# Kernel optimization log

Hardware: AMD Instinct MI355X
Metric: run time of the kernel (lower is better)

Reference implementation:

```python
import jax, jax.numpy as jnp
import numpy as np
import math

NUM_HEADS = 16
D_MODEL = 1024
LN_EPS = 1e-5


def _layer_norm(x, g, b):
    mu = jnp.mean(x, axis=-1, keepdims=True)
    var = jnp.mean((x - mu) ** 2, axis=-1, keepdims=True)
    return (x - mu) / jnp.sqrt(var + LN_EPS) * g + b


def setup_inputs() -> dict:
    key = jax.random.key(0)
    ks = jax.random.split(key, 12)
    B, H, W, d = 32, 16, 16, D_MODEL
    P, F = 64, 128
    s = 0.02
    return {
        "x": jax.random.normal(ks[0], (B, H, W, d), jnp.float32),
        "pattern_features": jax.random.normal(ks[1], (B, P, F), jnp.float32),
        "wq": jax.random.normal(ks[2], (d, d), jnp.float32) * s,
        "bq": jnp.zeros((d,), jnp.float32),
        "wk": jax.random.normal(ks[3], (d, d), jnp.float32) * s,
        "bk": jnp.zeros((d,), jnp.float32),
        "wv": jax.random.normal(ks[4], (d, d), jnp.float32) * s,
        "bv": jnp.zeros((d,), jnp.float32),
        "wo": jax.random.normal(ks[5], (d, d), jnp.float32) * s,
        "bo": jnp.zeros((d,), jnp.float32),
        "ln_g": jnp.ones((d,), jnp.float32),
        "ln_b": jnp.zeros((d,), jnp.float32),
    }


def reference(x, pattern_features, wq, bq, wk, bk, wv, bv, wo, bo, ln_g, ln_b):
    B, H, W, d = x.shape
    S = H * W
    nh = NUM_HEADS
    dk = d // nh
    x_seq = x.reshape(B, S, d)

    def proj(w, b):
        return (x_seq @ w.T + b).reshape(B, S, nh, dk).transpose(0, 2, 1, 3)  # (B,nh,S,dk)

    q, k, v = proj(wq, bq), proj(wk, bk), proj(wv, bv)
    scores = jnp.einsum("bhsd,bhtd->bhst", q, k) / math.sqrt(dk)  # (B,nh,S,S)

    # creative bias: diversity bonus on top-left min(S,64) block, same for all heads
    m = min(S, 64)
    sim = jnp.einsum("bpf,bqf->bpq", pattern_features, pattern_features)
    div = 1.0 - jax.nn.softmax(sim, axis=-1)  # (B,P,P)
    bias = jnp.zeros((B, nh, S, S), x.dtype)
    bias = bias.at[:, :, :m, :m].set(div[:, None, :m, :m] * 0.1)

    # faithful to torch: scores + bias.unsqueeze(0) -> rank-5 (1,B,nh,S,S)
    scores5 = scores[None] + bias[None]
    aw = jax.nn.softmax(scores5, axis=-1)
    attn = jnp.matmul(aw, v)  # (1,B,nh,S,dk) via broadcasting
    # faithful to torch transpose(1,2).view(B,S,d): row-major reshape of (1,nh,B,S,dk)
    attn = jnp.transpose(attn, (0, 2, 1, 3, 4)).reshape(B, S, d)

    out = attn @ wo.T + bo
    out = _layer_norm(out + x_seq, ln_g, ln_b)

    attention_weights = jax.nn.softmax(scores, axis=-1).mean(axis=1)  # (B,S,S)
    return out.reshape(B, H, W, d), attention_weights
```

## Files before the change

kernel.cpp:

```cpp
#include <hip/hip_runtime.h>

typedef unsigned short u16;
typedef unsigned int   u32;
typedef short bf16x8 __attribute__((ext_vector_type(8)));
typedef float f32x4  __attribute__((ext_vector_type(4)));

__device__ __forceinline__ float bf2f(u16 u){
  union { u32 u; float f; } c; c.u = ((u32)u) << 16; return c.f;
}
__device__ __forceinline__ u16 f2bf(float f){
  union { float f; u32 u; } c; c.f = f;
  u32 u = c.u + 0x7fffu + ((c.u >> 16) & 1u);
  return (u16)(u >> 16);
}

__device__ __forceinline__ void gload16(const u16* g, u16* l){
  __builtin_amdgcn_global_load_lds((const __attribute__((address_space(1))) u32*)g,
                                   (__attribute__((address_space(3))) u32*)l, 16, 0, 0);
}

__device__ __forceinline__ float waveRed(float v, int ismax){
  #pragma unroll
  for (int o = 32; o > 0; o >>= 1){
    float t = __shfl_xor(v, o, 64);
    v = ismax ? fmaxf(v, t) : (v + t);
  }
  return v;
}
__device__ __forceinline__ float blockRed(float v, int ismax, float* red, int tid){
  v = waveRed(v, ismax);
  __syncthreads();
  if ((tid & 63) == 0) red[tid >> 6] = v;
  __syncthreads();
  return ismax ? fmaxf(fmaxf(red[0], red[1]), fmaxf(red[2], red[3]))
               : (red[0] + red[1] + red[2] + red[3]);
}

__global__ __launch_bounds__(256)
void conv_x(const float* __restrict__ src, u16* __restrict__ dst){
  const size_t i = ((size_t)blockIdx.x * 256 + threadIdx.x) * 8;
  const float4 a = *(const float4*)(src + i);
  const float4 b = *(const float4*)(src + i + 4);
  uint4 o;
  o.x = (u32)f2bf(a.x) | ((u32)f2bf(a.y) << 16);
  o.y = (u32)f2bf(a.z) | ((u32)f2bf(a.w) << 16);
  o.z = (u32)f2bf(b.x) | ((u32)f2bf(b.y) << 16);
  o.w = (u32)f2bf(b.z) | ((u32)f2bf(b.w) << 16);
  *(uint4*)(dst + i) = o;
}

__global__ __launch_bounds__(256)
void conv_w4(const float* __restrict__ w0, const float* __restrict__ w1,
             const float* __restrict__ w2, const float* __restrict__ w3,
             u16* __restrict__ dst){
  const float* s = blockIdx.y == 0 ? w0 : (blockIdx.y == 1 ? w1 : (blockIdx.y == 2 ? w2 : w3));
  u16* d = dst + (size_t)blockIdx.y * 1048576;
  const size_t i = ((size_t)blockIdx.x * 256 + threadIdx.x) * 8;
  const float4 a = *(const float4*)(s + i);
  const float4 b = *(const float4*)(s + i + 4);
  uint4 o;
  o.x = (u32)f2bf(a.x) | ((u32)f2bf(a.y) << 16);
  o.y = (u32)f2bf(a.z) | ((u32)f2bf(a.w) << 16);
  o.z = (u32)f2bf(b.x) | ((u32)f2bf(b.y) << 16);
  o.w = (u32)f2bf(b.z) | ((u32)f2bf(b.w) << 16);
  *(uint4*)(d + i) = o;
}

__global__ __launch_bounds__(256)
void div_kernel(const float* __restrict__ pf, float* __restrict__ divp)
{
  __shared__ float pfs[64][129];
  __shared__ float svs[64][65];
  const int b = blockIdx.x;
  const int tid = threadIdx.x;
  const float* pb = pf + (size_t)b * 8192;
  for (int i = tid; i < 8192; i += 256) pfs[i >> 7][i & 127] = pb[i];
  __syncthreads();
  const int p = tid & 63, qg = tid >> 6;
  for (int qq = qg * 16; qq < qg * 16 + 16; ++qq){
    float a = 0.f;
    #pragma unroll 8
    for (int f = 0; f < 128; ++f) a += pfs[p][f] * pfs[qq][f];
    svs[p][qq] = a;
  }
  __syncthreads();
  if (tid < 64){
    float m = -1e30f;
    for (int qq = 0; qq < 64; ++qq) m = fmaxf(m, svs[tid][qq]);
    float s = 0.f;
    for (int qq = 0; qq < 64; ++qq){ const float e = __expf(svs[tid][qq] - m); svs[tid][qq] = e; s += e; }
    const float inv = 1.f / s;
    float* dr = divp + ((size_t)b * 64 + tid) * 64;
    for (int qq = 0; qq < 64; ++qq) dr[qq] = 0.1f * (1.f - svs[tid][qq] * inv);
  }
}

template<int MODE>
__global__ __launch_bounds__(256)
void gemm_lds(const u16* __restrict__ A, const u16* __restrict__ Wb,
              const float* __restrict__ bias0, const float* __restrict__ bias1,
              const float* __restrict__ bias2, void* __restrict__ outp)
{
  __shared__ u16 As[128 * 32];
  __shared__ u16 Bs[128 * 32];
  const int tid = threadIdx.x, lane = tid & 63, w = tid >> 6;
  const int wm = (w >> 1) * 64, wn = (w & 1) * 64;
  const int bm = blockIdx.x;
  int bn = blockIdx.y;
  const u16* Wp = Wb;
  const float* bias = bias0;
  float scale = 1.f;
  int wsel = 0;
  if (MODE == 0){
    wsel = bn >> 3; bn &= 7;
    Wp = Wb + (size_t)wsel * 1048576;
    bias = wsel == 0 ? bias0 : (wsel == 1 ? bias1 : bias2);
    if (wsel == 0) scale = 0.125f;
  }

  const f32x4 z = {0.f, 0.f, 0.f, 0.f};
  f32x4 acc[4][4];
  #pragma unroll
  for (int i = 0; i < 4; ++i)
    #pragma unroll
    for (int j = 0; j < 4; ++j) acc[i][j] = z;

  const int r4 = lane >> 2, c8 = (lane & 3) * 8;
  const int ca0 = w * 2, ca1 = w * 2 + 1;
  const u16* ga0 = A  + (size_t)(bm * 128 + ca0 * 16 + r4) * 1024 + c8;
  const u16* ga1 = A  + (size_t)(bm * 128 + ca1 * 16 + r4) * 1024 + c8;
  const u16* gb0 = Wp + (size_t)(bn * 128 + ca0 * 16 + r4) * 1024 + c8;
  const u16* gb1 = Wp + (size_t)(bn * 128 + ca1 * 16 + r4) * 1024 + c8;
  u16* la0 = As + ca0 * 512 + lane * 8;
  u16* la1 = As + ca1 * 512 + lane * 8;
  u16* lb0 = Bs + ca0 * 512 + lane * 8;
  u16* lb1 = Bs + ca1 * 512 + lane * 8;

  const int fr = lane & 15, q8 = (lane >> 4) * 8;
  for (int k0 = 0; k0 < 1024; k0 += 32){
    __syncthreads();
    gload16(ga0 + k0, la0);
    gload16(ga1 + k0, la1);
    gload16(gb0 + k0, lb0);
    gload16(gb1 + k0, lb1);
    __syncthreads();
    bf16x8 af[4], bfv[4];
    #pragma unroll
    for (int i = 0; i < 4; ++i) af[i]  = *(const bf16x8*)&As[(wm + i * 16 + fr) * 32 + q8];
    #pragma unroll
    for (int j = 0; j < 4; ++j) bfv[j] = *(const bf16x8*)&Bs[(wn + j * 16 + fr) * 32 + q8];
    #pragma unroll
    for (int i = 0; i < 4; ++i)
      #pragma unroll
      for (int j = 0; j < 4; ++j)
        acc[i][j] = __builtin_amdgcn_mfma_f32_16x16x32_bf16(af[i], bfv[j], acc[i][j], 0, 0, 0);
  }

  #pragma unroll
  for (int i = 0; i < 4; ++i){
    #pragma unroll
    for (int j = 0; j < 4; ++j){
      const int gr0 = bm * 128 + wm + i * 16 + ((lane >> 4) * 4);
      const int gc  = bn * 128 + wn + j * 16 + (lane & 15);
      const float bvv = bias[gc];
      #pragma unroll
      for (int r = 0; r < 4; ++r){
        const int gr = gr0 + r;
        const float val = (acc[i][j][r] + bvv) * scale;
        if (MODE == 0){
          const int b = gr >> 8, s = gr & 255, h = gc >> 6, kk = gc & 63;
          ((u16*)outp)[(size_t)wsel * 8388608 + (size_t)b * 262144 +
                       (size_t)h * 16384 + (size_t)s * 64 + kk] = f2bf(val);
        } else {
          ((float*)outp)[(size_t)gr * 1024 + gc] = val;
        }
      }
    }
  }
}

__global__ __launch_bounds__(256)
void attn_mfma(const u16* __restrict__ q, const u16* __restrict__ k,
               const u16* __restrict__ v, const float* __restrict__ divp,
               u16* __restrict__ attn_s)
{
  __shared__ u16 Vt[64][264];
  __shared__ u16 Ps[4][16][136];
  const int bh = blockIdx.x;
  const int b = bh >> 4, h = bh & 15;
  const int tid = threadIdx.x, lane = tid & 63, w = tid >> 6;
  const int quad = lane >> 4, l15 = lane & 15;
  const u16* kh = k + (size_t)bh * 16384;
  const u16* vh = v + (size_t)bh * 16384;
  const u16* qh = q + (size_t)bh * 16384;

  #pragma unroll
  for (int c = 0; c < 4; ++c){
    const int pidx = tid + c * 256;
    const int t2 = pidx & 127;
    const int n0 = (pidx >> 7) * 8;
    const uint4 a  = *(const uint4*)(vh + (2 * t2) * 64 + n0);
    const uint4 bb = *(const uint4*)(vh + (2 * t2 + 1) * 64 + n0);
    const u32 aa[4] = {a.x, a.y, a.z, a.w};
    const u32 bb4[4] = {bb.x, bb.y, bb.z, bb.w};
    #pragma unroll
    for (int j2 = 0; j2 < 4; ++j2){
      const u32 lo = aa[j2], hi = bb4[j2];
      *(u32*)&Vt[n0 + 2 * j2    ][2 * t2] = (lo & 0xffffu) | (hi << 16);
      *(u32*)&Vt[n0 + 2 * j2 + 1][2 * t2] = (lo >> 16) | (hi & 0xffff0000u);
    }
  }
  __syncthreads();

  const f32x4 z = {0.f, 0.f, 0.f, 0.f};
  const int bp = 2 * h + (b >> 4);
  for (int i = 0; i < 4; ++i){
    const int row0 = w * 64 + i * 16;
    const bf16x8 af0 = *(const bf16x8*)(qh + (size_t)(row0 + l15) * 64 + quad * 8);
    const bf16x8 af1 = *(const bf16x8*)(qh + (size_t)(row0 + l15) * 64 + 32 + quad * 8);
    f32x4 sc[16];
    #pragma unroll
    for (int ct = 0; ct < 16; ++ct){
      const bf16x8 b0 = *(const bf16x8*)(kh + (size_t)(ct * 16 + l15) * 64 + quad * 8);
      const bf16x8 b1 = *(const bf16x8*)(kh + (size_t)(ct * 16 + l15) * 64 + 32 + quad * 8);
      f32x4 a = __builtin_amdgcn_mfma_f32_16x16x32_bf16(af0, b0, z, 0, 0, 0);
      sc[ct]  = __builtin_amdgcn_mfma_f32_16x16x32_bf16(af1, b1, a, 0, 0, 0);
    }
    if (w == 0){
      const float* dv = divp + (size_t)b * 4096 + (size_t)(i * 16 + quad * 4) * 64 + l15;
      #pragma unroll
      for (int ct = 0; ct < 4; ++ct)
        #pragma unroll
        for (int rr = 0; rr < 4; ++rr)
          sc[ct][rr] += dv[rr * 64 + ct * 16];
    }
    float rs[4];
    #pragma unroll
    for (int rr = 0; rr < 4; ++rr){
      float m = sc[0][rr];
      #pragma unroll
      for (int ct = 1; ct < 16; ++ct) m = fmaxf(m, sc[ct][rr]);
      #pragma unroll
      for (int o = 1; o < 16; o <<= 1) m = fmaxf(m, __shfl_xor(m, o, 64));
      float s = 0.f;
      #pragma unroll
      for (int ct = 0; ct < 16; ++ct){
        const float e = __expf(sc[ct][rr] - m); sc[ct][rr] = e; s += e;
      }
      #pragma unroll
      for (int o = 1; o < 16; o <<= 1) s += __shfl_xor(s, o, 64);
      rs[rr] = 1.f / s;
    }
    f32x4 o4[4] = {z, z, z, z};
    #pragma unroll
    for (int half = 0; half < 2; ++half){
      #pragma unroll
      for (int ct = 0; ct < 8; ++ct)
        #pragma unroll
        for (int rr = 0; rr < 4; ++rr)
          Ps[w][quad * 4 + rr][ct * 16 + l15] = f2bf(sc[half * 8 + ct][rr] * rs[rr]);
      #pragma unroll
      for (int kc = 0; kc < 4; ++kc){
        const bf16x8 pa = *(const bf16x8*)&Ps[w][l15][kc * 32 + quad * 8];
        #pragma unroll
        for (int nt = 0; nt < 4; ++nt){
          const bf16x8 vb8 = *(const bf16x8*)&Vt[nt * 16 + l15][half * 128 + kc * 32 + quad * 8];
          o4[nt] = __builtin_amdgcn_mfma_f32_16x16x32_bf16(pa, vb8, o4[nt], 0, 0, 0);
        }
      }
    }
    const int sp = (b & 15) * 16 + (w * 4 + i);
    #pragma unroll
    for (int nt = 0; nt < 4; ++nt)
      #pragma unroll
      for (int rr = 0; rr < 4; ++rr){
        const int slo = quad * 4 + rr;
        const int cp = slo * 64 + nt * 16 + l15;
        attn_s[((size_t)bp * 256 + sp) * 1024 + cp] = f2bf(o4[nt][rr]);
      }
  }
}

__global__ __launch_bounds__(256)
void aw_kernel(const u16* __restrict__ q, const u16* __restrict__ k,
               float* __restrict__ aw)
{
  __shared__ float redm[16][4];
  __shared__ float reds[16][4];
  const int blk = blockIdx.x;
  const int b = blk >> 4, st = blk & 15;
  const int tid = threadIdx.x, lane = tid & 63, w = tid >> 6;
  const int quad = lane >> 4, l15 = lane & 15;
  const int rowb = st * 16;
  const f32x4 z = {0.f, 0.f, 0.f, 0.f};
  float awacc[4][4] = {};
  for (int h = 0; h < 16; ++h){
    const u16* kh = k + (((size_t)b * 16 + h) * 16384);
    const u16* qh = q + (((size_t)b * 16 + h) * 16384);
    const bf16x8 af0 = *(const bf16x8*)(qh + (size_t)(rowb + l15) * 64 + quad * 8);
    const bf16x8 af1 = *(const bf16x8*)(qh + (size_t)(rowb + l15) * 64 + 32 + quad * 8);
    f32x4 sc[4];
    #pragma unroll
    for (int j4 = 0; j4 < 4; ++j4){
      const int ct = w * 4 + j4;
      const bf16x8 b0 = *(const bf16x8*)(kh + (size_t)(ct * 16 + l15) * 64 + quad * 8);
      const bf16x8 b1 = *(const bf16x8*)(kh + (size_t)(ct * 16 + l15) * 64 + 32 + quad * 8);
      f32x4 a = __builtin_amdgcn_mfma_f32_16x16x32_bf16(af0, b0, z, 0, 0, 0);
      sc[j4]  = __builtin_amdgcn_mfma_f32_16x16x32_bf16(af1, b1, a, 0, 0, 0);
    }
    float pm[4];
    #pragma unroll
    for (int rr = 0; rr < 4; ++rr){
      float m = fmaxf(fmaxf(sc[0][rr], sc[1][rr]), fmaxf(sc[2][rr], sc[3][rr]));
      #pragma unroll
      for (int o = 1; o < 16; o <<= 1) m = fmaxf(m, __shfl_xor(m, o, 64));
      pm[rr] = m;
    }
    if (l15 == 0)
      #pragma unroll
      for (int rr = 0; rr < 4; ++rr) redm[quad * 4 + rr][w] = pm[rr];
    __syncthreads();
    float ps[4];
    #pragma unroll
    for (int rr = 0; rr < 4; ++rr){
      const int row = quad * 4 + rr;
      const float m = fmaxf(fmaxf(redm[row][0], redm[row][1]),
                            fmaxf(redm[row][2], redm[row][3]));
      float s = 0.f;
      #pragma unroll
      for (int j4 = 0; j4 < 4; ++j4){
        const float e = __expf(sc[j4][rr] - m); sc[j4][rr] = e; s += e;
      }
      #pragma unroll
      for (int o = 1; o < 16; o <<= 1) s += __shfl_xor(s, o, 64);
      ps[rr] = s;
    }
    if (l15 == 0)
      #pragma unroll
      for (int rr = 0; rr < 4; ++rr) reds[quad * 4 + rr][w] = ps[rr];
    __syncthreads();
    #pragma unroll
    for (int rr = 0; rr < 4; ++rr){
      const int row = quad * 4 + rr;
      const float inv = 1.f / (reds[row][0] + reds[row][1] + reds[row][2] + reds[row][3]);
      #pragma unroll
      for (int j4 = 0; j4 < 4; ++j4) awacc[j4][rr] += sc[j4][rr] * inv;
    }
  }
  const size_t base = (size_t)b * 65536;
  #pragma unroll
  for (int j4 = 0; j4 < 4; ++j4){
    const int col = (w * 4 + j4) * 16 + l15;
    #pragma unroll
    for (int rr = 0; rr < 4; ++rr){
      const int row = rowb + quad * 4 + rr;
      aw[base + (size_t)row * 256 + col] = awacc[j4][rr] * 0.0625f;
    }
  }
}

__global__ __launch_bounds__(256)
void ln_kernel(const float* __restrict__ y2, const float* __restrict__ x,
               const float* __restrict__ g, const float* __restrict__ bb,
               float* __restrict__ outp)
{
  __shared__ float red[4];
  const int r = blockIdx.x, tid = threadIdx.x;
  const float4 yv = ((const float4*)(y2 + (size_t)r * 1024))[tid];
  const float4 xv = ((const float4*)(x  + (size_t)r * 1024))[tid];
  const float v0 = yv.x + xv.x;
  const float v1 = yv.y + xv.y;
  const float v2 = yv.z + xv.z;
  const float v3 = yv.w + xv.w;
  const float ssum = blockRed(v0 + v1 + v2 + v3, 0, red, tid);
  const float mu = ssum * (1.f / 1024.f);
  const float d0 = v0 - mu, d1 = v1 - mu, d2 = v2 - mu, d3 = v3 - mu;
  const float sq = blockRed(d0 * d0 + d1 * d1 + d2 * d2 + d3 * d3, 0, red, tid);
  const float rstd = rsqrtf(sq * (1.f / 1024.f) + 1e-5f);
  const float4 gv = ((const float4*)g)[tid];
  const float4 bv = ((const float4*)bb)[tid];
  float4 o;
  o.x = d0 * rstd * gv.x + bv.x;
  o.y = d1 * rstd * gv.y + bv.y;
  o.z = d2 * rstd * gv.z + bv.z;
  o.w = d3 * rstd * gv.w + bv.w;
  ((float4*)(outp + (size_t)r * 1024))[tid] = o;
}

extern "C" void kernel_launch(void* const* d_in, const int* in_sizes, int n_in,
                              void* d_out, int out_size, void* d_ws, size_t ws_size,
                              hipStream_t stream)
{
  int ix = -1, ipf = -1, iw[4] = {-1,-1,-1,-1}, iv[6] = {-1,-1,-1,-1,-1,-1};
  int nw = 0, nv = 0;
  for (int i = 0; i < n_in; ++i){
    const int sz = in_sizes[i];
    if (sz == 8388608 && ix < 0) ix = i;
    else if (sz == 262144 && ipf < 0) ipf = i;
    else if (sz == 1048576 && nw < 4) iw[nw++] = i;
    else if (sz == 1024 && nv < 6) iv[nv++] = i;
  }
  if (ix < 0 || ipf < 0 || nw != 4 || nv != 6){
    ix = 0; ipf = 1; iw[0] = 2; iv[0] = 3; iw[1] = 4; iv[1] = 5;
    iw[2] = 6; iv[2] = 7; iw[3] = 8; iv[3] = 9; iv[4] = 10; iv[5] = 11;
  }

  const float* x   = (const float*)d_in[ix];
  const float* pf  = (const float*)d_in[ipf];
  const float* wq  = (const float*)d_in[iw[0]];
  const float* wk  = (const float*)d_in[iw[1]];
  const float* wv  = (const float*)d_in[iw[2]];
  const float* wo  = (const float*)d_in[iw[3]];
  const float* bq  = (const float*)d_in[iv[0]];
  const float* bk  = (const float*)d_in[iv[1]];
  const float* bv  = (const float*)d_in[iv[2]];
  const float* bo  = (const float*)d_in[iv[3]];
  const float* lng = (const float*)d_in[iv[4]];
  const float* lnb = (const float*)d_in[iv[5]];

  float* out0   = (float*)d_out;
  float* aw_out = out0 + 8388608;

  u16* x_bf = (u16*)d_out;
  u16* attn = x_bf + 8388608;
  u16* qkv    = (u16*)d_ws;
  float* divp = (float*)((char*)d_ws + (size_t)48 * 1048576);
  u16* warena = (u16*)((char*)d_ws + (size_t)49 * 1048576);
  float* y2   = (float*)d_ws;

  conv_x<<<4096, 256, 0, stream>>>(x, x_bf);
  conv_w4<<<dim3(512, 4), 256, 0, stream>>>(wq, wk, wv, wo, warena);
  div_kernel<<<32, 256, 0, stream>>>(pf, divp);

  gemm_lds<0><<<dim3(64, 24), 256, 0, stream>>>(x_bf, warena, bq, bk, bv, (void*)qkv);

  u16* qw = qkv, *kw = qkv + 8388608, *vw = qkv + 16777216;
  attn_mfma<<<512, 256, 0, stream>>>(qw, kw, vw, divp, attn);
  aw_kernel<<<512, 256, 0, stream>>>(qw, kw, aw_out);

  gemm_lds<1><<<dim3(64, 8), 256, 0, stream>>>(attn, warena + 3145728, bo, nullptr, nullptr, (void*)y2);
  ln_kernel<<<8192, 256, 0, stream>>>(y2, x, lng, lnb, out0);
}
```

Measured before the change: 330.8 us.

## Split attention blocks by row quarter and give each aw wave its own heads

The attention kernel now launches four blocks per (batch, head), each handling 64 query rows, instead of one block looping over 256 rows. This raises the grid from 512 to 2048 blocks for better CU occupancy, at the cost of each block redundantly transposing the full V tile into LDS. The averaged-weights kernel now has each wave process four heads over all 256 columns, which removes the per-head block-wide barriers. Per-wave partial sums are then combined through a 64KB LDS buffer, which may lower occupancy and raises register use (64 accumulators plus 64 score registers).

```diff
diff --git a/kernel.cpp b/kernel.cpp
--- a/kernel.cpp
+++ b/kernel.cpp
@@ -186,7 +186,8 @@
 {
   __shared__ u16 Vt[64][264];
   __shared__ u16 Ps[4][16][136];
-  const int bh = blockIdx.x;
+  const int blk = blockIdx.x;
+  const int bh = blk >> 2, rq = blk & 3;
   const int b = bh >> 4, h = bh & 15;
   const int tid = threadIdx.x, lane = tid & 63, w = tid >> 6;
   const int quad = lane >> 4, l15 = lane & 15;
@@ -214,148 +215,128 @@
 
   const f32x4 z = {0.f, 0.f, 0.f, 0.f};
   const int bp = 2 * h + (b >> 4);
-  for (int i = 0; i < 4; ++i){
-    const int row0 = w * 64 + i * 16;
-    const bf16x8 af0 = *(const bf16x8*)(qh + (size_t)(row0 + l15) * 64 + quad * 8);
-    const bf16x8 af1 = *(const bf16x8*)(qh + (size_t)(row0 + l15) * 64 + 32 + quad * 8);
-    f32x4 sc[16];
+  const int row0 = rq * 64 + w * 16;
+  const bf16x8 af0 = *(const bf16x8*)(qh + (size_t)(row0 + l15) * 64 + quad * 8);
+  const bf16x8 af1 = *(const bf16x8*)(qh + (size_t)(row0 + l15) * 64 + 32 + quad * 8);
+  f32x4 sc[16];
+  #pragma unroll
+  for (int ct = 0; ct < 16; ++ct){
+    const bf16x8 b0 = *(const bf16x8*)(kh + (size_t)(ct * 16 + l15) * 64 + quad * 8);
+    const bf16x8 b1 = *(const bf16x8*)(kh + (size_t)(ct * 16 + l15) * 64 + 32 + quad * 8);
+    f32x4 a = __builtin_amdgcn_mfma_f32_16x16x32_bf16(af0, b0, z, 0, 0, 0);
+    sc[ct]  = __builtin_amdgcn_mfma_f32_16x16x32_bf16(af1, b1, a, 0, 0, 0);
+  }
+  if (rq == 0){
+    const float* dv = divp + (size_t)b * 4096 + (size_t)(w * 16 + quad * 4) * 64 + l15;
+    #pragma unroll
+    for (int ct = 0; ct < 4; ++ct)
+      #pragma unroll
+      for (int rr = 0; rr < 4; ++rr)
+        sc[ct][rr] += dv[rr * 64 + ct * 16];
+  }
+  float rs[4];
+  #pragma unroll
+  for (int rr = 0; rr < 4; ++rr){
+    float m = sc[0][rr];
+    #pragma unroll
+    for (int ct = 1; ct < 16; ++ct) m = fmaxf(m, sc[ct][rr]);
+    #pragma unroll
+    for (int o = 1; o < 16; o <<= 1) m = fmaxf(m, __shfl_xor(m, o, 64));
+    float s = 0.f;
     #pragma unroll
     for (int ct = 0; ct < 16; ++ct){
-      const bf16x8 b0 = *(const bf16x8*)(kh + (size_t)(ct * 16 + l15) * 64 + quad * 8);
-      const bf16x8 b1 = *(const bf16x8*)(kh + (size_t)(ct * 16 + l15) * 64 + 32 + quad * 8);
-      f32x4 a = __builtin_amdgcn_mfma_f32_16x16x32_bf16(af0, b0, z, 0, 0, 0);
-      sc[ct]  = __builtin_amdgcn_mfma_f32_16x16x32_bf16(af1, b1, a, 0, 0, 0);
-    }
-    if (w == 0){
-      const float* dv = divp + (size_t)b * 4096 + (size_t)(i * 16 + quad * 4) * 64 + l15;
-      #pragma unroll
-      for (int ct = 0; ct < 4; ++ct)
-        #pragma unroll
-        for (int rr = 0; rr < 4; ++rr)
-          sc[ct][rr] += dv[rr * 64 + ct * 16];
-    }
-    float rs[4];
+      const float e = __expf(sc[ct][rr] - m); sc[ct][rr] = e; s += e;
+    }
+    #pragma unroll
+    for (int o = 1; o < 16; o <<= 1) s += __shfl_xor(s, o, 64);
+    rs[rr] = 1.f / s;
+  }
+  f32x4 o4[4] = {z, z, z, z};
+  #pragma unroll
+  for (int half = 0; half < 2; ++half){
+    #pragma unroll
+    for (int ct = 0; ct < 8; ++ct)
+      #pragma unroll
+      for (int rr = 0; rr < 4; ++rr)
+        Ps[w][quad * 4 + rr][ct * 16 + l15] = f2bf(sc[half * 8 + ct][rr] * rs[rr]);
+    #pragma unroll
+    for (int kc = 0; kc < 4; ++kc){
+      const bf16x8 pa = *(const bf16x8*)&Ps[w][l15][kc * 32 + quad * 8];
+      #pragma unroll
+      for (int nt = 0; nt < 4; ++nt){
+        const bf16x8 vb8 = *(const bf16x8*)&Vt[nt * 16 + l15][half * 128 + kc * 32 + quad * 8];
+        o4[nt] = __builtin_amdgcn_mfma_f32_16x16x32_bf16(pa, vb8, o4[nt], 0, 0, 0);
+      }
+    }
+  }
+  const int sp = (b & 15) * 16 + rq * 4 + w;
+  #pragma unroll
+  for (int nt = 0; nt < 4; ++nt)
     #pragma unroll
     for (int rr = 0; rr < 4; ++rr){
-      float m = sc[0][rr];
-      #pragma unroll
-      for (int ct = 1; ct < 16; ++ct) m = fmaxf(m, sc[ct][rr]);
-      #pragma unroll
-      for (int o = 1; o < 16; o <<= 1) m = fmaxf(m, __shfl_xor(m, o, 64));
-      float s = 0.f;
-      #pragma unroll
-      for (int ct = 0; ct < 16; ++ct){
-        const float e = __expf(sc[ct][rr] - m); sc[ct][rr] = e; s += e;
-      }
-      #pragma unroll
-      for (int o = 1; o < 16; o <<= 1) s += __shfl_xor(s, o, 64);
-      rs[rr] = 1.f / s;
-    }
-    f32x4 o4[4] = {z, z, z, z};
-    #pragma unroll
-    for (int half = 0; half < 2; ++half){
-      #pragma unroll
-      for (int ct = 0; ct < 8; ++ct)
-        #pragma unroll
-        for (int rr = 0; rr < 4; ++rr)
-          Ps[w][quad * 4 + rr][ct * 16 + l15] = f2bf(sc[half * 8 + ct][rr] * rs[rr]);
-      #pragma unroll
-      for (int kc = 0; kc < 4; ++kc){
-        const bf16x8 pa = *(const bf16x8*)&Ps[w][l15][kc * 32 + quad * 8];
-        #pragma unroll
-        for (int nt = 0; nt < 4; ++nt){
-          const bf16x8 vb8 = *(const bf16x8*)&Vt[nt * 16 + l15][half * 128 + kc * 32 + quad * 8];
-          o4[nt] = __builtin_amdgcn_mfma_f32_16x16x32_bf16(pa, vb8, o4[nt], 0, 0, 0);
-        }
-      }
-    }
-    const int sp = (b & 15) * 16 + (w * 4 + i);
-    #pragma unroll
-    for (int nt = 0; nt < 4; ++nt)
-      #pragma unroll
-      for (int rr = 0; rr < 4; ++rr){
-        const int slo = quad * 4 + rr;
-        const int cp = slo * 64 + nt * 16 + l15;
-        attn_s[((size_t)bp * 256 + sp) * 1024 + cp] = f2bf(o4[nt][rr]);
-      }
-  }
+      const int slo = quad * 4 + rr;
+      const int cp = slo * 64 + nt * 16 + l15;
+      attn_s[((size_t)bp * 256 + sp) * 1024 + cp] = f2bf(o4[nt][rr]);
+    }
 }
 
 __global__ __launch_bounds__(256)
 void aw_kernel(const u16* __restrict__ q, const u16* __restrict__ k,
                float* __restrict__ aw)
 {
-  __shared__ float redm[16][4];
-  __shared__ float reds[16][4];
+  __shared__ float Ws[4][16][258];
   const int blk = blockIdx.x;
   const int b = blk >> 4, st = blk & 15;
   const int tid = threadIdx.x, lane = tid & 63, w = tid >> 6;
   const int quad = lane >> 4, l15 = lane & 15;
   const int rowb = st * 16;
   const f32x4 z = {0.f, 0.f, 0.f, 0.f};
-  float awacc[4][4] = {};
-  for (int h = 0; h < 16; ++h){
+  float awacc[16][4] = {};
+  #pragma unroll
+  for (int hh = 0; hh < 4; ++hh){
+    const int h = w * 4 + hh;
     const u16* kh = k + (((size_t)b * 16 + h) * 16384);
     const u16* qh = q + (((size_t)b * 16 + h) * 16384);
     const bf16x8 af0 = *(const bf16x8*)(qh + (size_t)(rowb + l15) * 64 + quad * 8);
     const bf16x8 af1 = *(const bf16x8*)(qh + (size_t)(rowb + l15) * 64 + 32 + quad * 8);
-    f32x4 sc[4];
-    #pragma unroll
-    for (int j4 = 0; j4 < 4; ++j4){
-      const int ct = w * 4 + j4;
+    f32x4 sc[16];
+    #pragma unroll
+    for (int ct = 0; ct < 16; ++ct){
       const bf16x8 b0 = *(const bf16x8*)(kh + (size_t)(ct * 16 + l15) * 64 + quad * 8);
       const bf16x8 b1 = *(const bf16x8*)(kh + (size_t)(ct * 16 + l15) * 64 + 32 + quad * 8);
       f32x4 a = __builtin_amdgcn_mfma_f32_16x16x32_bf16(af0, b0, z, 0, 0, 0);
-      sc[j4]  = __builtin_amdgcn_mfma_f32_16x16x32_bf16(af1, b1, a, 0, 0, 0);
-    }
-    float pm[4];
+      sc[ct]  = __builtin_amdgcn_mfma_f32_16x16x32_bf16(af1, b1, a, 0, 0, 0);
+    }
     #pragma unroll
     for (int rr = 0; rr < 4; ++rr){
-      float m = fmaxf(fmaxf(sc[0][rr], sc[1][rr]), fmaxf(sc[2][rr], sc[3][rr]));
+      float m = sc[0][rr];
+      #pragma unroll
+      for (int ct = 1; ct < 16; ++ct) m = fmaxf(m, sc[ct][rr]);
       #pragma unroll
       for (int o = 1; o < 16; o <<= 1) m = fmaxf(m, __shfl_xor(m, o, 64));
-      pm[rr] = m;
-    }
-    if (l15 == 0)
-      #pragma unroll
-      for (int rr = 0; rr < 4; ++rr) redm[quad * 4 + rr][w] = pm[rr];
-    __syncthreads();
-    float ps[4];
-    #pragma unroll
-    for (int rr = 0; rr < 4; ++rr){
-      const int row = quad * 4 + rr;
-      const float m = fmaxf(fmaxf(redm[row][0], redm[row][1]),
-                            fmaxf(redm[row][2], redm[row][3]));
       float s = 0.f;
       #pragma unroll
-      for (int j4 = 0; j4 < 4; ++j4){
-        const float e = __expf(sc[j4][rr] - m); sc[j4][rr] = e; s += e;
+      for (int ct = 0; ct < 16; ++ct){
+        const float e = __expf(sc[ct][rr] - m); sc[ct][rr] = e; s += e;
       }
       #pragma unroll
       for (int o = 1; o < 16; o <<= 1) s += __shfl_xor(s, o, 64);
-      ps[rr] = s;
-    }
-    if (l15 == 0)
-      #pragma unroll
-      for (int rr = 0; rr < 4; ++rr) reds[quad * 4 + rr][w] = ps[rr];
-    __syncthreads();
-    #pragma unroll
-    for (int rr = 0; rr < 4; ++rr){
-      const int row = quad * 4 + rr;
-      const float inv = 1.f / (reds[row][0] + reds[row][1] + reds[row][2] + reds[row][3]);
-      #pragma unroll
-      for (int j4 = 0; j4 < 4; ++j4) awacc[j4][rr] += sc[j4][rr] * inv;
-    }
-  }
-  const size_t base = (size_t)b * 65536;
-  #pragma unroll
-  for (int j4 = 0; j4 < 4; ++j4){
-    const int col = (w * 4 + j4) * 16 + l15;
-    #pragma unroll
-    for (int rr = 0; rr < 4; ++rr){
-      const int row = rowb + quad * 4 + rr;
-      aw[base + (size_t)row * 256 + col] = awacc[j4][rr] * 0.0625f;
-    }
+      const float inv = 1.f / s;
+      #pragma unroll
+      for (int ct = 0; ct < 16; ++ct) awacc[ct][rr] += sc[ct][rr] * inv;
+    }
+  }
+  #pragma unroll
+  for (int ct = 0; ct < 16; ++ct)
+    #pragma unroll
+    for (int rr = 0; rr < 4; ++rr)
+      Ws[w][quad * 4 + rr][ct * 16 + l15] = awacc[ct][rr];
+  __syncthreads();
+  float* dst = aw + (size_t)b * 65536 + (size_t)rowb * 256;
+  for (int t = tid; t < 4096; t += 256){
+    const int r = t >> 8, c = t & 255;
+    dst[(size_t)r * 256 + c] =
+        (Ws[0][r][c] + Ws[1][r][c] + Ws[2][r][c] + Ws[3][r][c]) * 0.0625f;
   }
 }
 
@@ -435,7 +416,7 @@
   gemm_lds<0><<<dim3(64, 24), 256, 0, stream>>>(x_bf, warena, bq, bk, bv, (void*)qkv);
 
   u16* qw = qkv, *kw = qkv + 8388608, *vw = qkv + 16777216;
-  attn_mfma<<<512, 256, 0, stream>>>(qw, kw, vw, divp, attn);
+  attn_mfma<<<2048, 256, 0, stream>>>(qw, kw, vw, divp, attn);
   aw_kernel<<<512, 256, 0, stream>>>(qw, kw, aw_out);
 
   gemm_lds<1><<<dim3(64, 8), 256, 0, stream>>>(attn, warena + 3145728, bo, nullptr, nullptr, (void*)y2);
```

New measurement: 338.3 us. +2.3%, slower.
